# Performance work log

Hardware: AMD Instinct MI355X
Metric: run time of the kernel (lower is better)

Reference implementation:

```python
import jax, jax.numpy as jnp
import numpy as np

N_ATOMS = 21
SIG = 10.0
C = 0.0
STD = 1.0
Q = np.sqrt(5.0) / SIG  # Matern-5/2 length-scale factor


def setup_inputs() -> dict:
    key = jax.random.key(0)
    k1, k2, k3 = jax.random.split(key, 3)
    # geometries: scale so interatomic distances are O(1) and nonzero
    Rs = jax.random.normal(k1, (128, N_ATOMS, 3), dtype=jnp.float32) * 2.0
    # training descriptors are inverse distances -> positive, O(0.1..1)
    xs_train = jax.random.uniform(k2, (4096, 210), dtype=jnp.float32, minval=0.1, maxval=1.0)
    Jx_alphas = jax.random.normal(k3, (4096, 210), dtype=jnp.float32)
    return {"Rs": Rs, "xs_train": xs_train, "Jx_alphas": Jx_alphas}


def reference(Rs, xs_train, Jx_alphas):
    M, n = Rs.shape[0], Rs.shape[1]
    i, j = np.tril_indices(n, k=-1)  # static index sets

    # pairwise atom displacements and safe distances (diag masked, not inf)
    diffs = Rs[:, :, None, :] - Rs[:, None, :, :]            # [M,n,n,3]
    sq = jnp.sum(diffs * diffs, axis=-1)                      # [M,n,n]
    eye = jnp.eye(n, dtype=Rs.dtype)
    dists = jnp.sqrt(sq + eye)                                # diag -> 1 (safe)

    # coulomb_matrix descriptor: inverse distances on strict lower triangle
    xs = 1.0 / dists[:, i, j]                                 # [M,D]

    # distances in descriptor space to all (perm-expanded) training points
    x_diffs = Q * xs[:, None, :] - Q * xs_train               # [M,T,D]
    x_dists = jnp.linalg.norm(x_diffs, axis=-1)               # [M,T]

    exp_xs = (5.0 / (3.0 * SIG * SIG)) * jnp.exp(-x_dists)    # kernel weights
    dot = jnp.einsum('mtd,td->mt', x_diffs, Jx_alphas)        # [M,T]
    exp1 = exp_xs * (1.0 + x_dists)

    F1 = jnp.einsum('mt,mtd->md', exp_xs * dot, x_diffs)      # [M,D]
    F2 = exp1 @ Jx_alphas                                     # [M,D]
    Fs_x = (F1 - F2) * STD

    # expand_tril: symmetric full matrix with zero diagonal
    full = jnp.zeros((M, n, n), dtype=Rs.dtype)
    full = full.at[:, i, j].set(Fs_x).at[:, j, i].set(Fs_x)

    # zero out diagonal contribution (original divides by inf there)
    inv_d3 = (1.0 - eye) / (dists ** 3)
    Fs = jnp.einsum('mab,mabc->mbc', full * inv_d3, diffs)    # [M,n,3]

    Es = C + (jnp.sum(exp1 * dot, axis=-1) / Q) * STD         # [M]
    return Es, Fs
```

## Files before the change

kernel.cpp:

```cpp
#include <hip/hip_runtime.h>
#include <hip/hip_bf16.h>

#define MM 128
#define NA 21
#define DD 210
#define DP 224
#define TT 4096
#define NC 64
#define CHT 64
#define XPAD 20

#define QF   0.22360679774997896f
#define Q2F  0.05f
#define K0E  0.016666666666666666f
#define INVQ 4.47213595499958f

#define OFF_TRP  0
#define OFF_JXP  (OFF_TRP + TT*DP)
#define OFF_TRPT (OFF_JXP + TT*DP)
#define OFF_JXPT (OFF_TRPT + DP*TT)
#define OFF_XSP  (OFF_JXPT + DP*TT)
#define OFF_NT   (OFF_XSP + MM*DP)
#define OFF_CT   (OFF_NT + TT)
#define OFF_NM   (OFF_CT + TT)
#define OFF_S1P  (OFF_NM + MM)
#define OFF_EP   (OFF_S1P + NC*MM)
#define OFF_P1   (OFF_EP + NC*MM)
#define OFF_P2   (OFF_P1 + NC*MM*DP)

__global__ __launch_bounds__(256) void k0_prep(
        const float* __restrict__ tr, const float* __restrict__ jx,
        const float* __restrict__ Rs,
        float* __restrict__ trp, float* __restrict__ jxp,
        float* __restrict__ trpT, float* __restrict__ jxpT,
        float* __restrict__ nt, float* __restrict__ ct,
        float* __restrict__ xsp, float* __restrict__ nmg) {
    __shared__ float S1[16][225];
    __shared__ float S2[16][225];
    int b = blockIdx.x, tid = threadIdx.x;

    if (b < 256) {
        int t0 = b * 16;
        for (int i = tid; i < 16 * 224; i += 256) {
            int t = i / 224, d = i - t * 224;
            float v1 = 0.f, v2 = 0.f;
            if (d < DD) { v1 = tr[(t0 + t) * DD + d]; v2 = jx[(t0 + t) * DD + d]; }
            S1[t][d] = v1; S2[t][d] = v2;
            trp[(t0 + t) * DP + d] = v1;
            jxp[(t0 + t) * DP + d] = v2;
        }
        __syncthreads();
        if (tid < 64) {
            int t = tid & 15, seg = tid >> 4;
            float sn = 0.f, sc = 0.f;
            int d0 = seg * 56;
            for (int d = d0; d < d0 + 56; ++d) {
                float v1 = S1[t][d];
                sn = fmaf(v1, v1, sn);
                sc = fmaf(v1, S2[t][d], sc);
            }
            sn += __shfl_xor(sn, 16); sn += __shfl_xor(sn, 32);
            sc += __shfl_xor(sc, 16); sc += __shfl_xor(sc, 32);
            if (seg == 0) { nt[t0 + t] = sn; ct[t0 + t] = sc; }
        }
        for (int i = tid; i < 224 * 16; i += 256) {
            int d = i >> 4, t = i & 15;
            trpT[d * TT + t0 + t] = S1[t][d];
            jxpT[d * TT + t0 + t] = S2[t][d];
        }
    } else {
        int m = b - 256;
        float* Rl  = &S1[0][0];
        float* red = &S2[0][0];
        if (tid < NA * 3) Rl[tid] = Rs[m * NA * 3 + tid];
        __syncthreads();
        float v = 0.f;
        if (tid < DP) {
            float x = 0.f;
            if (tid < DD) {
                int d = tid;
                int a = (int)((1.0f + sqrtf(8.0f * (float)d + 1.0f)) * 0.5f);
                while (a * (a - 1) / 2 > d) --a;
                while ((a + 1) * a / 2 <= d) ++a;
                int bb = d - a * (a - 1) / 2;
                float dx = Rl[a * 3 + 0] - Rl[bb * 3 + 0];
                float dy = Rl[a * 3 + 1] - Rl[bb * 3 + 1];
                float dz = Rl[a * 3 + 2] - Rl[bb * 3 + 2];
                x = 1.0f / sqrtf(dx * dx + dy * dy + dz * dz);
            }
            xsp[m * DP + tid] = x;
            v = x * x;
        }
        #pragma unroll
        for (int off = 32; off >= 1; off >>= 1) v += __shfl_xor(v, off);
        if ((tid & 63) == 0) red[tid >> 6] = v;
        __syncthreads();
        if (tid == 0) nmg[m] = red[0] + red[1] + red[2] + red[3];
    }
}

#define PA_LOAD(bt, bj, KK) do { \
    _Pragma("unroll") \
    for (int u = 0; u < 8; ++u) { \
        bt[u] = tb[(KK + u) * TT]; \
        bj[u] = jb[(KK + u) * TT]; \
    } } while (0)

#define PA_FMA(bt, bj, KK) do { \
    _Pragma("unroll") \
    for (int u = 0; u < 8; ++u) { \
        float4 a = *(const float4*)&xst[(KK + u) * XPAD + my4]; \
        g1[0] = fmaf(a.x, bt[u], g1[0]); \
        g1[1] = fmaf(a.y, bt[u], g1[1]); \
        g1[2] = fmaf(a.z, bt[u], g1[2]); \
        g1[3] = fmaf(a.w, bt[u], g1[3]); \
        g2[0] = fmaf(a.x, bj[u], g2[0]); \
        g2[1] = fmaf(a.y, bj[u], g2[1]); \
        g2[2] = fmaf(a.z, bj[u], g2[2]); \
        g2[3] = fmaf(a.w, bj[u], g2[3]); \
    } } while (0)

#define PB_LOAD(xa1, xa2, T) do { \
    xa1[0] = *(const float4*)&trp[(t0 + (T)) * DP + d0]; \
    xa1[1] = *(const float4*)&trp[(t0 + (T) + 1) * DP + d0]; \
    xa2[0] = *(const float4*)&jxp[(t0 + (T)) * DP + d0]; \
    xa2[1] = *(const float4*)&jxp[(t0 + (T) + 1) * DP + d0]; } while (0)

#define PB_FMA(xa1, xa2, T) do { \
    _Pragma("unroll") \
    for (int i = 0; i < 4; ++i) { \
        float2 w1p = *(const float2*)&Wl1[my4 + i][(T)]; \
        float2 w2p = *(const float2*)&Wl2[my4 + i][(T)]; \
        a1[i].x = fmaf(w1p.x, xa1[0].x, fmaf(w1p.y, xa1[1].x, a1[i].x)); \
        a1[i].y = fmaf(w1p.x, xa1[0].y, fmaf(w1p.y, xa1[1].y, a1[i].y)); \
        a1[i].z = fmaf(w1p.x, xa1[0].z, fmaf(w1p.y, xa1[1].z, a1[i].z)); \
        a1[i].w = fmaf(w1p.x, xa1[0].w, fmaf(w1p.y, xa1[1].w, a1[i].w)); \
        a2[i].x = fmaf(w2p.x, xa2[0].x, fmaf(w2p.y, xa2[1].x, a2[i].x)); \
        a2[i].y = fmaf(w2p.x, xa2[0].y, fmaf(w2p.y, xa2[1].y, a2[i].y)); \
        a2[i].z = fmaf(w2p.x, xa2[0].z, fmaf(w2p.y, xa2[1].z, a2[i].z)); \
        a2[i].w = fmaf(w2p.x, xa2[0].w, fmaf(w2p.y, xa2[1].w, a2[i].w)); \
    } } while (0)

__global__ __launch_bounds__(256) void k23_fused(
        const float* __restrict__ trp, const float* __restrict__ jxp,
        const float* __restrict__ trpT, const float* __restrict__ jxpT,
        const float* __restrict__ xsp, const float* __restrict__ nt,
        const float* __restrict__ ct, const float* __restrict__ nm,
        float* __restrict__ S1P, float* __restrict__ EP,
        float* __restrict__ P1, float* __restrict__ P2) {
    __shared__ __align__(16) float xst[224 * XPAD];
    __shared__ __align__(16) float Wl1[16][CHT];
    __shared__ __align__(16) float Wl2[16][CHT];
    int tid = threadIdx.x;
    int c = blockIdx.x, m0 = blockIdx.y * 16;
    int t0 = c * CHT;
    int tx = tid & 63, wq = tid >> 6, my4 = wq * 4;
    int mq = m0 + my4;

    for (int i = tid; i < 16 * 224; i += 256) {
        int m = i / 224, k = i - m * 224;
        xst[k * XPAD + m] = xsp[(m0 + m) * DP + k];
    }
    __syncthreads();

    float g1[4] = {0.f, 0.f, 0.f, 0.f};
    float g2[4] = {0.f, 0.f, 0.f, 0.f};
    const float* tb = trpT + t0 + tx;
    const float* jb = jxpT + t0 + tx;
    {
        float p0t[8], p0j[8], p1t[8], p1j[8];
        PA_LOAD(p0t, p0j, 0);
        int k = 0;
        for (; k < DP - 16; k += 16) {
            PA_LOAD(p1t, p1j, k + 8);
            PA_FMA(p0t, p0j, k);
            PA_LOAD(p0t, p0j, k + 16);
            PA_FMA(p1t, p1j, k + 8);
        }
        PA_LOAD(p1t, p1j, DP - 8);
        PA_FMA(p0t, p0j, DP - 16);
        PA_FMA(p1t, p1j, DP - 8);
    }

    float ntv = nt[t0 + tx], ctv = ct[t0 + tx];
    float s1l[4], el[4];
    #pragma unroll
    for (int i = 0; i < 4; ++i) {
        float nmv = nm[mq + i];
        float d2 = Q2F * (nmv + ntv - 2.f * g1[i]);
        float xd = sqrtf(fmaxf(d2, 0.f));
        float e  = K0E * __expf(-xd);
        float dv = QF * (g2[i] - ctv);
        float w1 = e * dv;
        float w2 = e * (1.f + xd);
        Wl1[my4 + i][tx] = w1;
        Wl2[my4 + i][tx] = w2;
        s1l[i] = w1;
        el[i]  = w2 * dv;
    }
    #pragma unroll
    for (int off = 32; off >= 1; off >>= 1) {
        #pragma unroll
        for (int i = 0; i < 4; ++i) {
            s1l[i] += __shfl_xor(s1l[i], off);
            el[i]  += __shfl_xor(el[i], off);
        }
    }
    if (tx == 0) {
        #pragma unroll
        for (int i = 0; i < 4; ++i) {
            S1P[c * MM + mq + i] = s1l[i];
            EP [c * MM + mq + i] = el[i];
        }
    }

    int d0 = 4 * (tx < 56 ? tx : 55);
    bool act = (tx < 56);
    float4 a1[4], a2[4];
    #pragma unroll
    for (int i = 0; i < 4; ++i) { a1[i] = {0.f,0.f,0.f,0.f}; a2[i] = {0.f,0.f,0.f,0.f}; }
    {
        float4 xa1[2], xa2[2], xb1[2], xb2[2];
        PB_LOAD(xa1, xa2, 0);
        int g = 0;
        for (; g < 30; g += 2) {
            PB_LOAD(xb1, xb2, (g + 1) * 2);
            PB_FMA(xa1, xa2, g * 2);
            PB_LOAD(xa1, xa2, (g + 2) * 2);
            PB_FMA(xb1, xb2, (g + 1) * 2);
        }
        PB_LOAD(xb1, xb2, 62);
        PB_FMA(xa1, xa2, 60);
        PB_FMA(xb1, xb2, 62);
    }
    if (act) {
        #pragma unroll
        for (int i = 0; i < 4; ++i) {
            *(float4*)&P1[((size_t)c * MM + mq + i) * DP + d0] = a1[i];
            *(float4*)&P2[((size_t)c * MM + mq + i) * DP + d0] = a2[i];
        }
    }
}

__global__ __launch_bounds__(1024) void k4_final(
        const float* __restrict__ Rs, const float* __restrict__ xsp,
        const float* __restrict__ P1, const float* __restrict__ P2,
        const float* __restrict__ S1P, const float* __restrict__ EP,
        float* __restrict__ out) {
    int m = blockIdx.x, tid = threadIdx.x;
    int q = tid >> 8, r = tid & 255;
    __shared__ float fred1[4][256];
    __shared__ float fred2[4][256];
    __shared__ float fxs[DD];
    __shared__ float Rl[64];
    __shared__ float sE[2];
    if (tid < NA * 3) Rl[tid] = Rs[m * NA * 3 + tid];
    if (r < DD) {
        float pa = 0.f, pb = 0.f;
        #pragma unroll 8
        for (int cc = q * 16; cc < q * 16 + 16; ++cc) {
            pa += P1[((size_t)cc * MM + m) * DP + r];
            pb += P2[((size_t)cc * MM + m) * DP + r];
        }
        fred1[q][r] = pa;
        fred2[q][r] = pb;
    }
    if (tid < 64) {
        float s = S1P[tid * MM + m];
        float e = EP [tid * MM + m];
        #pragma unroll
        for (int off = 32; off >= 1; off >>= 1) {
            s += __shfl_xor(s, off);
            e += __shfl_xor(e, off);
        }
        if (tid == 0) { sE[0] = s; sE[1] = e; }
    }
    __syncthreads();
    if (tid < DD) {
        float pa = fred1[0][tid] + fred1[1][tid] + fred1[2][tid] + fred1[3][tid];
        float pb = fred2[0][tid] + fred2[1][tid] + fred2[2][tid] + fred2[3][tid];
        fxs[tid] = QF * xsp[m * DP + tid] * sE[0] - QF * pa - pb;
    }
    __syncthreads();
    if (tid < NA * 3) {
        int b = tid / 3, c = tid - b * 3;
        float acc = 0.f;
        #pragma unroll
        for (int a = 0; a < NA; ++a) {
            if (a == b) continue;
            int hi = a > b ? a : b, lo = a > b ? b : a;
            int d = hi * (hi - 1) / 2 + lo;
            float dx = Rl[a * 3 + 0] - Rl[b * 3 + 0];
            float dy = Rl[a * 3 + 1] - Rl[b * 3 + 1];
            float dz = Rl[a * 3 + 2] - Rl[b * 3 + 2];
            float r2 = dx * dx + dy * dy + dz * dz;
            float ir = 1.0f / sqrtf(r2);
            float w = fxs[d] * ir * ir * ir;
            float comp = (c == 0) ? dx : ((c == 1) ? dy : dz);
            acc = fmaf(w, comp, acc);
        }
        out[MM + m * NA * 3 + tid] = acc;
    }
    if (tid == 0) out[m] = sE[1] * INVQ;
}

extern "C" void kernel_launch(void* const* d_in, const int* in_sizes, int n_in,
                              void* d_out, int out_size, void* d_ws, size_t ws_size,
                              hipStream_t stream) {
    const float* Rs = (const float*)d_in[0];
    const float* tr = (const float*)d_in[1];
    const float* jx = (const float*)d_in[2];
    float* out = (float*)d_out;
    float* ws = (float*)d_ws;

    float* trp  = ws + OFF_TRP;
    float* jxp  = ws + OFF_JXP;
    float* trpT = ws + OFF_TRPT;
    float* jxpT = ws + OFF_JXPT;
    float* xsp  = ws + OFF_XSP;
    float* nt   = ws + OFF_NT;
    float* ct   = ws + OFF_CT;
    float* nm   = ws + OFF_NM;
    float* S1P  = ws + OFF_S1P;
    float* EP   = ws + OFF_EP;
    float* P1   = ws + OFF_P1;
    float* P2   = ws + OFF_P2;

    k0_prep<<<384, 256, 0, stream>>>(tr, jx, Rs, trp, jxp, trpT, jxpT, nt, ct, xsp, nm);
    k23_fused<<<dim3(NC, MM / 16), 256, 0, stream>>>(trp, jxp, trpT, jxpT, xsp, nt, ct, nm, S1P, EP, P1, P2);
    k4_final<<<MM, 1024, 0, stream>>>(Rs, xsp, P1, P2, S1P, EP, out);
}
```

Baseline: 52.58 us.

## Store transposed training data in float4-interleaved layout for vector loads

The transposed copies of the training descriptors and Jx_alphas are now written as groups of four consecutive descriptor elements per training point, so the fused kernel's first phase fetches them with float4 loads instead of eight strided scalar loads. The prep kernel now handles 32 training rows per block, so fewer blocks are launched, and it writes the transposed output as float4 stores. This is meant to cut global load instruction count and improve coalescing. The cost is larger shared-memory tiles in the prep kernel and fewer prep blocks.

```diff
diff --git a/kernel.cpp b/kernel.cpp
--- a/kernel.cpp
+++ b/kernel.cpp
@@ -15,33 +15,33 @@
 #define K0E  0.016666666666666666f
 #define INVQ 4.47213595499958f
 
-#define OFF_TRP  0
-#define OFF_JXP  (OFF_TRP + TT*DP)
-#define OFF_TRPT (OFF_JXP + TT*DP)
-#define OFF_JXPT (OFF_TRPT + DP*TT)
-#define OFF_XSP  (OFF_JXPT + DP*TT)
-#define OFF_NT   (OFF_XSP + MM*DP)
-#define OFF_CT   (OFF_NT + TT)
-#define OFF_NM   (OFF_CT + TT)
-#define OFF_S1P  (OFF_NM + MM)
-#define OFF_EP   (OFF_S1P + NC*MM)
-#define OFF_P1   (OFF_EP + NC*MM)
-#define OFF_P2   (OFF_P1 + NC*MM*DP)
+#define OFF_TRP   0
+#define OFF_JXP   (OFF_TRP + TT*DP)
+#define OFF_TRPT4 (OFF_JXP + TT*DP)
+#define OFF_JXPT4 (OFF_TRPT4 + DP*TT)
+#define OFF_XSP   (OFF_JXPT4 + DP*TT)
+#define OFF_NT    (OFF_XSP + MM*DP)
+#define OFF_CT    (OFF_NT + TT)
+#define OFF_NM    (OFF_CT + TT)
+#define OFF_S1P   (OFF_NM + MM)
+#define OFF_EP    (OFF_S1P + NC*MM)
+#define OFF_P1    (OFF_EP + NC*MM)
+#define OFF_P2    (OFF_P1 + NC*MM*DP)
 
 __global__ __launch_bounds__(256) void k0_prep(
         const float* __restrict__ tr, const float* __restrict__ jx,
         const float* __restrict__ Rs,
         float* __restrict__ trp, float* __restrict__ jxp,
-        float* __restrict__ trpT, float* __restrict__ jxpT,
+        float* __restrict__ trpT4, float* __restrict__ jxpT4,
         float* __restrict__ nt, float* __restrict__ ct,
         float* __restrict__ xsp, float* __restrict__ nmg) {
-    __shared__ float S1[16][225];
-    __shared__ float S2[16][225];
+    __shared__ __align__(16) float S1[32][228];
+    __shared__ __align__(16) float S2[32][228];
     int b = blockIdx.x, tid = threadIdx.x;
 
-    if (b < 256) {
-        int t0 = b * 16;
-        for (int i = tid; i < 16 * 224; i += 256) {
+    if (b < 128) {
+        int t0 = b * 32;
+        for (int i = tid; i < 32 * 224; i += 256) {
             int t = i / 224, d = i - t * 224;
             float v1 = 0.f, v2 = 0.f;
             if (d < DD) { v1 = tr[(t0 + t) * DD + d]; v2 = jx[(t0 + t) * DD + d]; }
@@ -51,25 +51,27 @@
         }
         __syncthreads();
         if (tid < 64) {
-            int t = tid & 15, seg = tid >> 4;
+            int t = tid & 31, h = tid >> 5;
             float sn = 0.f, sc = 0.f;
-            int d0 = seg * 56;
-            for (int d = d0; d < d0 + 56; ++d) {
+            int d0 = h * 112;
+            for (int d = d0; d < d0 + 112; ++d) {
                 float v1 = S1[t][d];
                 sn = fmaf(v1, v1, sn);
                 sc = fmaf(v1, S2[t][d], sc);
             }
-            sn += __shfl_xor(sn, 16); sn += __shfl_xor(sn, 32);
-            sc += __shfl_xor(sc, 16); sc += __shfl_xor(sc, 32);
-            if (seg == 0) { nt[t0 + t] = sn; ct[t0 + t] = sc; }
-        }
-        for (int i = tid; i < 224 * 16; i += 256) {
-            int d = i >> 4, t = i & 15;
-            trpT[d * TT + t0 + t] = S1[t][d];
-            jxpT[d * TT + t0 + t] = S2[t][d];
+            sn += __shfl_xor(sn, 32);
+            sc += __shfl_xor(sc, 32);
+            if (h == 0) { nt[t0 + t] = sn; ct[t0 + t] = sc; }
+        }
+        for (int i = tid; i < 56 * 32; i += 256) {
+            int kq = i >> 5, t = i & 31;
+            float4 v1 = *(const float4*)&S1[t][kq * 4];
+            float4 v2 = *(const float4*)&S2[t][kq * 4];
+            *(float4*)&trpT4[((size_t)kq * TT + t0 + t) * 4] = v1;
+            *(float4*)&jxpT4[((size_t)kq * TT + t0 + t) * 4] = v2;
         }
     } else {
-        int m = b - 256;
+        int m = b - 128;
         float* Rl  = &S1[0][0];
         float* red = &S2[0][0];
         if (tid < NA * 3) Rl[tid] = Rs[m * NA * 3 + tid];
@@ -100,11 +102,14 @@
 }
 
 #define PA_LOAD(bt, bj, KK) do { \
-    _Pragma("unroll") \
-    for (int u = 0; u < 8; ++u) { \
-        bt[u] = tb[(KK + u) * TT]; \
-        bj[u] = jb[(KK + u) * TT]; \
-    } } while (0)
+    float4 q0 = *(const float4*)&trpT4[((size_t)((KK) >> 2) * TT + tq) * 4]; \
+    float4 q1 = *(const float4*)&trpT4[((size_t)(((KK) >> 2) + 1) * TT + tq) * 4]; \
+    float4 r0 = *(const float4*)&jxpT4[((size_t)((KK) >> 2) * TT + tq) * 4]; \
+    float4 r1 = *(const float4*)&jxpT4[((size_t)(((KK) >> 2) + 1) * TT + tq) * 4]; \
+    bt[0] = q0.x; bt[1] = q0.y; bt[2] = q0.z; bt[3] = q0.w; \
+    bt[4] = q1.x; bt[5] = q1.y; bt[6] = q1.z; bt[7] = q1.w; \
+    bj[0] = r0.x; bj[1] = r0.y; bj[2] = r0.z; bj[3] = r0.w; \
+    bj[4] = r1.x; bj[5] = r1.y; bj[6] = r1.z; bj[7] = r1.w; } while (0)
 
 #define PA_FMA(bt, bj, KK) do { \
     _Pragma("unroll") \
@@ -143,7 +148,7 @@
 
 __global__ __launch_bounds__(256) void k23_fused(
         const float* __restrict__ trp, const float* __restrict__ jxp,
-        const float* __restrict__ trpT, const float* __restrict__ jxpT,
+        const float* __restrict__ trpT4, const float* __restrict__ jxpT4,
         const float* __restrict__ xsp, const float* __restrict__ nt,
         const float* __restrict__ ct, const float* __restrict__ nm,
         float* __restrict__ S1P, float* __restrict__ EP,
@@ -156,6 +161,7 @@
     int t0 = c * CHT;
     int tx = tid & 63, wq = tid >> 6, my4 = wq * 4;
     int mq = m0 + my4;
+    int tq = t0 + tx;
 
     for (int i = tid; i < 16 * 224; i += 256) {
         int m = i / 224, k = i - m * 224;
@@ -165,8 +171,6 @@
 
     float g1[4] = {0.f, 0.f, 0.f, 0.f};
     float g2[4] = {0.f, 0.f, 0.f, 0.f};
-    const float* tb = trpT + t0 + tx;
-    const float* jb = jxpT + t0 + tx;
     {
         float p0t[8], p0j[8], p1t[8], p1j[8];
         PA_LOAD(p0t, p0j, 0);
@@ -182,7 +186,7 @@
         PA_FMA(p1t, p1j, DP - 8);
     }
 
-    float ntv = nt[t0 + tx], ctv = ct[t0 + tx];
+    float ntv = nt[tq], ctv = ct[tq];
     float s1l[4], el[4];
     #pragma unroll
     for (int i = 0; i < 4; ++i) {
@@ -313,20 +317,20 @@
     float* out = (float*)d_out;
     float* ws = (float*)d_ws;
 
-    float* trp  = ws + OFF_TRP;
-    float* jxp  = ws + OFF_JXP;
-    float* trpT = ws + OFF_TRPT;
-    float* jxpT = ws + OFF_JXPT;
-    float* xsp  = ws + OFF_XSP;
-    float* nt   = ws + OFF_NT;
-    float* ct   = ws + OFF_CT;
-    float* nm   = ws + OFF_NM;
-    float* S1P  = ws + OFF_S1P;
-    float* EP   = ws + OFF_EP;
-    float* P1   = ws + OFF_P1;
-    float* P2   = ws + OFF_P2;
-
-    k0_prep<<<384, 256, 0, stream>>>(tr, jx, Rs, trp, jxp, trpT, jxpT, nt, ct, xsp, nm);
-    k23_fused<<<dim3(NC, MM / 16), 256, 0, stream>>>(trp, jxp, trpT, jxpT, xsp, nt, ct, nm, S1P, EP, P1, P2);
+    float* trp   = ws + OFF_TRP;
+    float* jxp   = ws + OFF_JXP;
+    float* trpT4 = ws + OFF_TRPT4;
+    float* jxpT4 = ws + OFF_JXPT4;
+    float* xsp   = ws + OFF_XSP;
+    float* nt    = ws + OFF_NT;
+    float* ct    = ws + OFF_CT;
+    float* nm    = ws + OFF_NM;
+    float* S1P   = ws + OFF_S1P;
+    float* EP    = ws + OFF_EP;
+    float* P1    = ws + OFF_P1;
+    float* P2    = ws + OFF_P2;
+
+    k0_prep<<<256, 256, 0, stream>>>(tr, jx, Rs, trp, jxp, trpT4, jxpT4, nt, ct, xsp, nm);
+    k23_fused<<<dim3(NC, MM / 16), 256, 0, stream>>>(trp, jxp, trpT4, jxpT4, xsp, nt, ct, nm, S1P, EP, P1, P2);
     k4_final<<<MM, 1024, 0, stream>>>(Rs, xsp, P1, P2, S1P, EP, out);
 }
```

New measurement: 55.48 us. 1.06x slower.

## Split fused kernel reductions across two thread halves with shared-memory combine

Applied to the files above, without the earlier changes.

Doubles the block size of the fused kernel to 512 threads. The extra four waves split the K dimension of the first dot-product phase and the T dimension of the second accumulation phase, and partial sums are combined through a reused shared-memory buffer. This aims to halve per-thread serial work and raise occupancy and latency hiding with only 512 blocks on the device. In exchange it adds extra syncthreads, shared-memory round trips for the partials, and idle threads during the weight computation.

```diff
diff --git a/kernel.cpp b/kernel.cpp
--- a/kernel.cpp
+++ b/kernel.cpp
@@ -121,16 +121,16 @@
     } } while (0)
 
 #define PB_LOAD(xa1, xa2, T) do { \
-    xa1[0] = *(const float4*)&trp[(t0 + (T)) * DP + d0]; \
-    xa1[1] = *(const float4*)&trp[(t0 + (T) + 1) * DP + d0]; \
-    xa2[0] = *(const float4*)&jxp[(t0 + (T)) * DP + d0]; \
-    xa2[1] = *(const float4*)&jxp[(t0 + (T) + 1) * DP + d0]; } while (0)
+    xa1[0] = *(const float4*)&trp[(TB + (T)) * DP + d0]; \
+    xa1[1] = *(const float4*)&trp[(TB + (T) + 1) * DP + d0]; \
+    xa2[0] = *(const float4*)&jxp[(TB + (T)) * DP + d0]; \
+    xa2[1] = *(const float4*)&jxp[(TB + (T) + 1) * DP + d0]; } while (0)
 
 #define PB_FMA(xa1, xa2, T) do { \
     _Pragma("unroll") \
     for (int i = 0; i < 4; ++i) { \
-        float2 w1p = *(const float2*)&Wl1[my4 + i][(T)]; \
-        float2 w2p = *(const float2*)&Wl2[my4 + i][(T)]; \
+        float2 w1p = *(const float2*)&Wl1f[(my4 + i) * 64 + tb0 + (T)]; \
+        float2 w2p = *(const float2*)&Wl2f[(my4 + i) * 64 + tb0 + (T)]; \
         a1[i].x = fmaf(w1p.x, xa1[0].x, fmaf(w1p.y, xa1[1].x, a1[i].x)); \
         a1[i].y = fmaf(w1p.x, xa1[0].y, fmaf(w1p.y, xa1[1].y, a1[i].y)); \
         a1[i].z = fmaf(w1p.x, xa1[0].z, fmaf(w1p.y, xa1[1].z, a1[i].z)); \
@@ -141,23 +141,26 @@
         a2[i].w = fmaf(w2p.x, xa2[0].w, fmaf(w2p.y, xa2[1].w, a2[i].w)); \
     } } while (0)
 
-__global__ __launch_bounds__(256) void k23_fused(
+__global__ __launch_bounds__(512) void k23_fused(
         const float* __restrict__ trp, const float* __restrict__ jxp,
         const float* __restrict__ trpT, const float* __restrict__ jxpT,
         const float* __restrict__ xsp, const float* __restrict__ nt,
         const float* __restrict__ ct, const float* __restrict__ nm,
         float* __restrict__ S1P, float* __restrict__ EP,
         float* __restrict__ P1, float* __restrict__ P2) {
-    __shared__ __align__(16) float xst[224 * XPAD];
-    __shared__ __align__(16) float Wl1[16][CHT];
-    __shared__ __align__(16) float Wl2[16][CHT];
+    __shared__ __align__(16) float smem[9216];
+    float* xst  = smem;
+    float* Wl1f = smem + 7168;
+    float* Wl2f = smem + 8192;
     int tid = threadIdx.x;
     int c = blockIdx.x, m0 = blockIdx.y * 16;
     int t0 = c * CHT;
-    int tx = tid & 63, wq = tid >> 6, my4 = wq * 4;
+    int tx = tid & 63, wq = tid >> 6;
+    int mw = wq & 3, kh = wq >> 2;
+    int my4 = mw * 4;
     int mq = m0 + my4;
 
-    for (int i = tid; i < 16 * 224; i += 256) {
+    for (int i = tid; i < 16 * 224; i += 512) {
         int m = i / 224, k = i - m * 224;
         xst[k * XPAD + m] = xsp[(m0 + m) * DP + k];
     }
@@ -168,54 +171,72 @@
     const float* tb = trpT + t0 + tx;
     const float* jb = jxpT + t0 + tx;
     {
+        int kb = kh * 112;
         float p0t[8], p0j[8], p1t[8], p1j[8];
-        PA_LOAD(p0t, p0j, 0);
-        int k = 0;
-        for (; k < DP - 16; k += 16) {
+        PA_LOAD(p0t, p0j, kb);
+        for (int k = kb; k < kb + 96; k += 16) {
             PA_LOAD(p1t, p1j, k + 8);
             PA_FMA(p0t, p0j, k);
             PA_LOAD(p0t, p0j, k + 16);
             PA_FMA(p1t, p1j, k + 8);
         }
-        PA_LOAD(p1t, p1j, DP - 8);
-        PA_FMA(p0t, p0j, DP - 16);
-        PA_FMA(p1t, p1j, DP - 8);
-    }
-
-    float ntv = nt[t0 + tx], ctv = ct[t0 + tx];
-    float s1l[4], el[4];
-    #pragma unroll
-    for (int i = 0; i < 4; ++i) {
-        float nmv = nm[mq + i];
-        float d2 = Q2F * (nmv + ntv - 2.f * g1[i]);
-        float xd = sqrtf(fmaxf(d2, 0.f));
-        float e  = K0E * __expf(-xd);
-        float dv = QF * (g2[i] - ctv);
-        float w1 = e * dv;
-        float w2 = e * (1.f + xd);
-        Wl1[my4 + i][tx] = w1;
-        Wl2[my4 + i][tx] = w2;
-        s1l[i] = w1;
-        el[i]  = w2 * dv;
-    }
-    #pragma unroll
-    for (int off = 32; off >= 1; off >>= 1) {
+        PA_LOAD(p1t, p1j, kb + 104);
+        PA_FMA(p0t, p0j, kb + 96);
+        PA_FMA(p1t, p1j, kb + 104);
+    }
+    __syncthreads();
+
+    float* Gc1 = smem;
+    float* Gc2 = smem + 1024;
+    if (kh == 1) {
         #pragma unroll
         for (int i = 0; i < 4; ++i) {
-            s1l[i] += __shfl_xor(s1l[i], off);
-            el[i]  += __shfl_xor(el[i], off);
-        }
-    }
-    if (tx == 0) {
+            Gc1[(my4 + i) * 64 + tx] = g1[i];
+            Gc2[(my4 + i) * 64 + tx] = g2[i];
+        }
+    }
+    __syncthreads();
+    if (kh == 0) {
+        float ntv = nt[t0 + tx], ctv = ct[t0 + tx];
+        float s1l[4], el[4];
         #pragma unroll
         for (int i = 0; i < 4; ++i) {
-            S1P[c * MM + mq + i] = s1l[i];
-            EP [c * MM + mq + i] = el[i];
-        }
-    }
+            float g1s = g1[i] + Gc1[(my4 + i) * 64 + tx];
+            float g2s = g2[i] + Gc2[(my4 + i) * 64 + tx];
+            float nmv = nm[mq + i];
+            float d2 = Q2F * (nmv + ntv - 2.f * g1s);
+            float xd = sqrtf(fmaxf(d2, 0.f));
+            float e  = K0E * __expf(-xd);
+            float dv = QF * (g2s - ctv);
+            float w1 = e * dv;
+            float w2 = e * (1.f + xd);
+            Wl1f[(my4 + i) * 64 + tx] = w1;
+            Wl2f[(my4 + i) * 64 + tx] = w2;
+            s1l[i] = w1;
+            el[i]  = w2 * dv;
+        }
+        #pragma unroll
+        for (int off = 32; off >= 1; off >>= 1) {
+            #pragma unroll
+            for (int i = 0; i < 4; ++i) {
+                s1l[i] += __shfl_xor(s1l[i], off);
+                el[i]  += __shfl_xor(el[i], off);
+            }
+        }
+        if (tx == 0) {
+            #pragma unroll
+            for (int i = 0; i < 4; ++i) {
+                S1P[c * MM + mq + i] = s1l[i];
+                EP [c * MM + mq + i] = el[i];
+            }
+        }
+    }
+    __syncthreads();
 
     int d0 = 4 * (tx < 56 ? tx : 55);
     bool act = (tx < 56);
+    int tb0 = kh * 32;
+    int TB  = t0 + tb0;
     float4 a1[4], a2[4];
     #pragma unroll
     for (int i = 0; i < 4; ++i) { a1[i] = {0.f,0.f,0.f,0.f}; a2[i] = {0.f,0.f,0.f,0.f}; }
@@ -223,19 +244,34 @@
         float4 xa1[2], xa2[2], xb1[2], xb2[2];
         PB_LOAD(xa1, xa2, 0);
         int g = 0;
-        for (; g < 30; g += 2) {
+        for (; g < 14; g += 2) {
             PB_LOAD(xb1, xb2, (g + 1) * 2);
             PB_FMA(xa1, xa2, g * 2);
             PB_LOAD(xa1, xa2, (g + 2) * 2);
             PB_FMA(xb1, xb2, (g + 1) * 2);
         }
-        PB_LOAD(xb1, xb2, 62);
-        PB_FMA(xa1, xa2, 60);
-        PB_FMA(xb1, xb2, 62);
-    }
-    if (act) {
+        PB_LOAD(xb1, xb2, 30);
+        PB_FMA(xa1, xa2, 28);
+        PB_FMA(xb1, xb2, 30);
+    }
+
+    float* Pc1 = smem;
+    float* Pc2 = smem + 3584;
+    if (kh == 1) {
         #pragma unroll
         for (int i = 0; i < 4; ++i) {
+            *(float4*)&Pc1[(my4 + i) * 224 + d0] = a1[i];
+            *(float4*)&Pc2[(my4 + i) * 224 + d0] = a2[i];
+        }
+    }
+    __syncthreads();
+    if (kh == 0 && act) {
+        #pragma unroll
+        for (int i = 0; i < 4; ++i) {
+            float4 q1 = *(const float4*)&Pc1[(my4 + i) * 224 + d0];
+            float4 q2 = *(const float4*)&Pc2[(my4 + i) * 224 + d0];
+            a1[i].x += q1.x; a1[i].y += q1.y; a1[i].z += q1.z; a1[i].w += q1.w;
+            a2[i].x += q2.x; a2[i].y += q2.y; a2[i].z += q2.z; a2[i].w += q2.w;
             *(float4*)&P1[((size_t)c * MM + mq + i) * DP + d0] = a1[i];
             *(float4*)&P2[((size_t)c * MM + mq + i) * DP + d0] = a2[i];
         }
@@ -327,6 +363,6 @@
     float* P2   = ws + OFF_P2;
 
     k0_prep<<<384, 256, 0, stream>>>(tr, jx, Rs, trp, jxp, trpT, jxpT, nt, ct, xsp, nm);
-    k23_fused<<<dim3(NC, MM / 16), 256, 0, stream>>>(trp, jxp, trpT, jxpT, xsp, nt, ct, nm, S1P, EP, P1, P2);
+    k23_fused<<<dim3(NC, MM / 16), 512, 0, stream>>>(trp, jxp, trpT, jxpT, xsp, nt, ct, nm, S1P, EP, P1, P2);
     k4_final<<<MM, 1024, 0, stream>>>(Rs, xsp, P1, P2, S1P, EP, out);
 }
```

Result: slower. 55.06 us (+4.7%).
